# Kernel optimization log

Hardware: AMD Instinct MI355X
Metric: run time of the kernel (lower is better)

Reference implementation:

```python
import jax, jax.numpy as jnp
import numpy as np

EPS = 1e-5

def sage_conv(x, edge_index, w_l, b_l, w_r):
    # PyG SAGEConv with mean aggregation: lin_l(mean of source-neighbor feats per dst) + lin_r(x)
    n = x.shape[0]
    src, dst = edge_index[0], edge_index[1]
    agg = jax.ops.segment_sum(x[src], dst, num_segments=n)  # [N, d]
    deg = jax.ops.segment_sum(jnp.ones((edge_index.shape[1],), x.dtype), dst, num_segments=n)
    agg = agg / jnp.maximum(deg, 1.0)[:, None]
    return agg @ w_l + b_l + x @ w_r

def batchnorm_eval(x, gamma, beta, mean, var):
    return (x - mean) * (gamma * jax.lax.rsqrt(var + EPS)) + beta

def setup_inputs() -> dict:
    key = jax.random.key(0)
    ks = jax.random.split(key, 12)
    N, E, D, H, O = 10000, 160000, 512, 512, 256
    inp = {
        'x': jax.random.normal(ks[0], (N, D), jnp.float32),
        'edge_index': jax.random.randint(ks[1], (2, E), 0, N, jnp.int32),
        'w_l1': jax.random.normal(ks[2], (D, H), jnp.float32) * (1.0 / np.sqrt(D)),
        'b1': jnp.zeros((H,), jnp.float32),
        'w_r1': jax.random.normal(ks[3], (D, H), jnp.float32) * (1.0 / np.sqrt(D)),
        'bn1_gamma': jnp.ones((H,), jnp.float32),
        'bn1_beta': jnp.zeros((H,), jnp.float32),
        'bn1_mean': jax.random.normal(ks[4], (H,), jnp.float32) * 0.1,
        'bn1_var': jax.random.uniform(ks[5], (H,), jnp.float32, 0.5, 1.5),
        'w_l2': jax.random.normal(ks[6], (H, H), jnp.float32) * (1.0 / np.sqrt(H)),
        'b2': jnp.zeros((H,), jnp.float32),
        'w_r2': jax.random.normal(ks[7], (H, H), jnp.float32) * (1.0 / np.sqrt(H)),
        'bn2_gamma': jnp.ones((H,), jnp.float32),
        'bn2_beta': jnp.zeros((H,), jnp.float32),
        'bn2_mean': jax.random.normal(ks[8], (H,), jnp.float32) * 0.1,
        'bn2_var': jax.random.uniform(ks[9], (H,), jnp.float32, 0.5, 1.5),
        'w_l3': jax.random.normal(ks[10], (H, O), jnp.float32) * (1.0 / np.sqrt(H)),
        'b3': jnp.zeros((O,), jnp.float32),
        'w_r3': jax.random.normal(ks[11], (H, O), jnp.float32) * (1.0 / np.sqrt(H)),
    }
    return inp

def reference(x, edge_index, w_l1, b1, w_r1, bn1_gamma, bn1_beta, bn1_mean, bn1_var,
              w_l2, b2, w_r2, bn2_gamma, bn2_beta, bn2_mean, bn2_var,
              w_l3, b3, w_r3):
    # Layer 1: SAGEConv -> BN (eval) -> ReLU (dropout is identity in eval)
    h = sage_conv(x, edge_index, w_l1, b1, w_r1)
    h = jax.nn.relu(batchnorm_eval(h, bn1_gamma, bn1_beta, bn1_mean, bn1_var))
    # Layer 2
    h = sage_conv(h, edge_index, w_l2, b2, w_r2)
    h = jax.nn.relu(batchnorm_eval(h, bn2_gamma, bn2_beta, bn2_mean, bn2_var))
    # Layer 3 (no BN/ReLU)
    return sage_conv(h, edge_index, w_l3, b3, w_r3)
```

## Files before the change

### kernel.cpp

```cpp
#include <hip/hip_runtime.h>

#define NNODE 10000
#define NEDGE 160000

using frag8 = __attribute__((ext_vector_type(8))) short;
using f32x4 = __attribute__((ext_vector_type(4))) float;

__device__ __forceinline__ unsigned short f2bf(float f) {
    union { float f; unsigned u; } v; v.f = f;
    unsigned r = (v.u + 0x7fffu + ((v.u >> 16) & 1u)) >> 16;
    return (unsigned short)r;
}
__device__ __forceinline__ float bf2f(unsigned short s) {
    union { unsigned u; float f; } v; v.u = ((unsigned)s) << 16; return v.f;
}

__global__ __launch_bounds__(1024) void k_scan(const int* __restrict__ deg,
                                               int* __restrict__ rs,
                                               int* __restrict__ cur, int n, int total) {
    const int tid = threadIdx.x;
    const int CH = 10;
    const int base = tid * CH;
    int vals[CH];
    int tsum = 0;
#pragma unroll
    for (int j = 0; j < CH; j++) {
        int v = (base + j < n) ? deg[base + j] : 0;
        vals[j] = v; tsum += v;
    }
    const int lane = tid & 63, wid = tid >> 6;
    int x = tsum;
#pragma unroll
    for (int d = 1; d < 64; d <<= 1) {
        int y = __shfl_up(x, d, 64);
        if (lane >= d) x += y;
    }
    __shared__ int wt[16];
    if (lane == 63) wt[wid] = x;
    __syncthreads();
    if (tid == 0) {
        int c = 0;
#pragma unroll
        for (int k = 0; k < 16; k++) { int t = wt[k]; wt[k] = c; c += t; }
    }
    __syncthreads();
    int run = wt[wid] + x - tsum;
#pragma unroll
    for (int j = 0; j < CH; j++) {
        if (base + j < n) { rs[base + j] = run; cur[base + j] = run; }
        run += vals[j];
    }
    if (tid == 0) rs[n] = total;
}

__global__ void k_fill(const int* __restrict__ src, const int* __restrict__ dst,
                       int E, int* __restrict__ cur, int* __restrict__ csr) {
    int e = blockIdx.x * 256 + threadIdx.x;
    if (e < E) {
        int p = atomicAdd(&cur[dst[e]], 1);
        csr[p] = src[e];
    }
}

__global__ __launch_bounds__(256) void k_prep(
    const float* __restrict__ x, unsigned short* __restrict__ xb,
    const float* __restrict__ wl1, const float* __restrict__ wr1,
    const float* __restrict__ wl2, const float* __restrict__ wr2,
    const float* __restrict__ wl3, const float* __restrict__ wr3,
    unsigned short* __restrict__ bt1, unsigned short* __restrict__ bt2,
    unsigned short* __restrict__ bt3,
    const float* __restrict__ b1, const float* __restrict__ g1, const float* __restrict__ be1,
    const float* __restrict__ m1, const float* __restrict__ v1,
    const float* __restrict__ b2, const float* __restrict__ g2, const float* __restrict__ be2,
    const float* __restrict__ m2, const float* __restrict__ v2,
    const float* __restrict__ b3,
    float* __restrict__ sc1, float* __restrict__ sh1,
    float* __restrict__ sc2, float* __restrict__ sh2,
    float* __restrict__ sc3, float* __restrict__ sh3,
    const int* __restrict__ dstI, int* __restrict__ deg) {
    const int b = blockIdx.x, tid = threadIdx.x;
    if (b < 5000) {
        int i = b * 256 + tid;
        float4 f = ((const float4*)x)[i];
        ushort4 o;
        o.x = f2bf(f.x); o.y = f2bf(f.y); o.z = f2bf(f.z); o.w = f2bf(f.w);
        ((ushort4*)xb)[i] = o;
        return;
    }
    if (b >= 6281) {
        int e = (b - 6281) * 256 + tid;
        if (e < NEDGE) atomicAdd(&deg[dstI[e]], 1);
        return;
    }
    if (b == 6280) {
        for (int t = tid; t < 512; t += 256) {
            float s1 = g1[t] * rsqrtf(v1[t] + 1e-5f);
            sc1[t] = s1; sh1[t] = (b1[t] - m1[t]) * s1 + be1[t];
            float s2 = g2[t] * rsqrtf(v2[t] + 1e-5f);
            sc2[t] = s2; sh2[t] = (b2[t] - m2[t]) * s2 + be2[t];
        }
        if (tid < 256) { sc3[tid] = 1.0f; sh3[tid] = b3[tid]; }
        return;
    }
    __shared__ float t[32][33];
    int tj = b - 5000;
    const float* srcp; unsigned short* dstp; int C, koff, ntilesN;
    if (tj < 1024) {
        int job = tj >> 8; int tile = tj & 255; C = 512; ntilesN = 16;
        srcp = (job == 0) ? wl1 : (job == 1) ? wr1 : (job == 2) ? wl2 : wr2;
        dstp = (job < 2) ? bt1 : bt2; koff = (job & 1) * 512;
        tj = tile;
    } else {
        int jj = tj - 1024; int job = jj >> 7; int tile = jj & 127; C = 256; ntilesN = 8;
        srcp = (job == 0) ? wl3 : wr3; dstp = bt3; koff = job * 512;
        tj = tile;
    }
    int k0 = (tj / ntilesN) * 32, c0 = (tj % ntilesN) * 32;
    int tx = tid & 31, ty = tid >> 5;
#pragma unroll
    for (int q = 0; q < 4; q++)
        t[ty + 8 * q][tx] = srcp[(long)(k0 + ty + 8 * q) * C + c0 + tx];
    __syncthreads();
#pragma unroll
    for (int q = 0; q < 4; q++)
        dstp[(long)(c0 + ty + 8 * q) * 1024 + koff + k0 + tx] = f2bf(t[tx][ty + 8 * q]);
}

__global__ __launch_bounds__(64) void k_agg(const unsigned short* __restrict__ S,
                                            const int* __restrict__ rs, const int* __restrict__ csr,
                                            unsigned short* __restrict__ outb) {
    const int n = blockIdx.x;
    const int c = blockIdx.y * 256 + threadIdx.x * 4;
    const int s = rs[n], e = rs[n + 1];
    float a0 = 0.f, a1 = 0.f, a2 = 0.f, a3 = 0.f;
    int i = s;
    for (; i + 4 <= e; i += 4) {
        int r0 = csr[i], r1 = csr[i + 1], r2 = csr[i + 2], r3 = csr[i + 3];
        uint2 u0 = *(const uint2*)(S + (long)r0 * 512 + c);
        uint2 u1 = *(const uint2*)(S + (long)r1 * 512 + c);
        uint2 u2 = *(const uint2*)(S + (long)r2 * 512 + c);
        uint2 u3 = *(const uint2*)(S + (long)r3 * 512 + c);
        a0 += bf2f((unsigned short)(u0.x & 0xffffu)); a1 += bf2f((unsigned short)(u0.x >> 16));
        a2 += bf2f((unsigned short)(u0.y & 0xffffu)); a3 += bf2f((unsigned short)(u0.y >> 16));
        a0 += bf2f((unsigned short)(u1.x & 0xffffu)); a1 += bf2f((unsigned short)(u1.x >> 16));
        a2 += bf2f((unsigned short)(u1.y & 0xffffu)); a3 += bf2f((unsigned short)(u1.y >> 16));
        a0 += bf2f((unsigned short)(u2.x & 0xffffu)); a1 += bf2f((unsigned short)(u2.x >> 16));
        a2 += bf2f((unsigned short)(u2.y & 0xffffu)); a3 += bf2f((unsigned short)(u2.y >> 16));
        a0 += bf2f((unsigned short)(u3.x & 0xffffu)); a1 += bf2f((unsigned short)(u3.x >> 16));
        a2 += bf2f((unsigned short)(u3.y & 0xffffu)); a3 += bf2f((unsigned short)(u3.y >> 16));
    }
    for (; i < e; i++) {
        uint2 u = *(const uint2*)(S + (long)csr[i] * 512 + c);
        a0 += bf2f((unsigned short)(u.x & 0xffffu)); a1 += bf2f((unsigned short)(u.x >> 16));
        a2 += bf2f((unsigned short)(u.y & 0xffffu)); a3 += bf2f((unsigned short)(u.y >> 16));
    }
    const int cnt = e - s;
    const float inv = 1.f / (float)(cnt > 1 ? cnt : 1);
    uint2 o;
    o.x = (unsigned)f2bf(a0 * inv) | ((unsigned)f2bf(a1 * inv) << 16);
    o.y = (unsigned)f2bf(a2 * inv) | ((unsigned)f2bf(a3 * inv) << 16);
    *(uint2*)(outb + (long)n * 512 + c) = o;
}

template <int MODE, int NOUT>
__global__ __launch_bounds__(256, 2) void k_gemm(const unsigned short* __restrict__ Agg,
                                                 const unsigned short* __restrict__ Self,
                                                 const unsigned short* __restrict__ Bt,
                                                 const float* __restrict__ sc, const float* __restrict__ sh,
                                                 unsigned short* __restrict__ hout, float* __restrict__ fout,
                                                 int M) {
    constexpr int NT = NOUT / 128;
    constexpr int QSH = (NT == 4) ? 5 : 4;
    const int b = blockIdx.x;
    const int X = b & 7;
    const int q = (b >> 3) & (NT - 1);
    const int g = b >> QSH;
    const int m0 = (g * 8 + X) * 128;
    if (m0 >= M) return;
    const int n0 = q * 128;

    __shared__ __align__(16) short As[2][128 * 64];
    __shared__ __align__(16) short Bs[2][128 * 64];
    const int tid = threadIdx.x;
    const int w = tid >> 6, lane = tid & 63;
    const int wm = (w >> 1) * 64, wn = (w & 1) * 64;
    const int fr = lane & 15, fq = lane >> 4, sw = fr & 7;
    const int srow = w * 8 + (lane >> 3);
    const int scol = (((lane & 7) ^ (lane >> 3)) * 8);
    const int ldsOff = w * 8 * 64;

    f32x4 acc[4][4];
#pragma unroll
    for (int i = 0; i < 4; i++)
#pragma unroll
        for (int j = 0; j < 4; j++)
#pragma unroll
            for (int r = 0; r < 4; r++) acc[i][j][r] = 0.f;

    auto issue = [&](int t, int buf) {
        const short* abase = (const short*)((t < 8) ? Agg : Self);
        const int kk = (t & 7) * 64;
        const int k0 = t * 64;
#pragma unroll
        for (int cch = 0; cch < 4; cch++) {
            __builtin_amdgcn_global_load_lds(
                (const __attribute__((address_space(1))) void*)(abase + (long)(m0 + cch * 32 + srow) * 512 + kk + scol),
                (__attribute__((address_space(3))) void*)(&As[buf][ldsOff + cch * 32 * 64]), 16, 0, 0);
            __builtin_amdgcn_global_load_lds(
                (const __attribute__((address_space(1))) void*)((const short*)Bt + (long)(n0 + cch * 32 + srow) * 1024 + k0 + scol),
                (__attribute__((address_space(3))) void*)(&Bs[buf][ldsOff + cch * 32 * 64]), 16, 0, 0);
        }
    };

    issue(0, 0);
#pragma unroll
    for (int t = 0; t < 16; t++) {
        const int cur = t & 1;
        __syncthreads();
        if (t < 15) issue(t + 1, cur ^ 1);
#pragma unroll
        for (int ks = 0; ks < 2; ks++) {
            frag8 af[4], bf[4];
#pragma unroll
            for (int i = 0; i < 4; i++)
                af[i] = *(const frag8*)(&As[cur][(wm + i * 16 + fr) * 64 + (((ks * 4 + fq) ^ sw) * 8)]);
#pragma unroll
            for (int j = 0; j < 4; j++)
                bf[j] = *(const frag8*)(&Bs[cur][(wn + j * 16 + fr) * 64 + (((ks * 4 + fq) ^ sw) * 8)]);
#pragma unroll
            for (int i = 0; i < 4; i++)
#pragma unroll
                for (int j = 0; j < 4; j++)
                    acc[i][j] = __builtin_amdgcn_mfma_f32_16x16x32_bf16(af[i], bf[j], acc[i][j], 0, 0, 0);
        }
    }

    float scj[4], shj[4];
#pragma unroll
    for (int j = 0; j < 4; j++) {
        int col = n0 + wn + j * 16 + fr;
        scj[j] = sc[col]; shj[j] = sh[col];
    }
#pragma unroll
    for (int i = 0; i < 4; i++) {
        int rowb = m0 + wm + i * 16 + fq * 4;
#pragma unroll
        for (int j = 0; j < 4; j++) {
            int col = n0 + wn + j * 16 + fr;
#pragma unroll
            for (int r = 0; r < 4; r++) {
                int row = rowb + r;
                if (row < M) {
                    float y = acc[i][j][r] * scj[j] + shj[j];
                    if constexpr (MODE == 0) {
                        y = fmaxf(y, 0.f);
                        hout[(long)row * 512 + col] = f2bf(y);
                    } else {
                        fout[(long)row * NOUT + col] = y;
                    }
                }
            }
        }
    }
}

extern "C" void kernel_launch(void* const* d_in, const int* in_sizes, int n_in,
                              void* d_out, int out_size, void* d_ws, size_t ws_size,
                              hipStream_t stream) {
    const float* x    = (const float*)d_in[0];
    const int*   ei   = (const int*)d_in[1];
    const float* w_l1 = (const float*)d_in[2];
    const float* b1   = (const float*)d_in[3];
    const float* w_r1 = (const float*)d_in[4];
    const float* g1   = (const float*)d_in[5];
    const float* be1  = (const float*)d_in[6];
    const float* m1   = (const float*)d_in[7];
    const float* v1   = (const float*)d_in[8];
    const float* w_l2 = (const float*)d_in[9];
    const float* b2   = (const float*)d_in[10];
    const float* w_r2 = (const float*)d_in[11];
    const float* g2   = (const float*)d_in[12];
    const float* be2  = (const float*)d_in[13];
    const float* m2   = (const float*)d_in[14];
    const float* v2   = (const float*)d_in[15];
    const float* w_l3 = (const float*)d_in[16];
    const float* b3   = (const float*)d_in[17];
    const float* w_r3 = (const float*)d_in[18];
    float* out = (float*)d_out;

    const int N = NNODE, E = NEDGE;
    const int* srcI = ei;
    const int* dstI = ei + E;

    char* w = (char*)d_ws;
    auto alloc = [&](size_t bytes) { void* p = (void*)w; w += (bytes + 255) & ~(size_t)255; return p; };
    int* deg = (int*)alloc((size_t)N * 4);
    int* rs  = (int*)alloc((size_t)(N + 1) * 4);
    int* cur = (int*)alloc((size_t)N * 4);
    int* csr = (int*)alloc((size_t)E * 4);
    unsigned short* xb   = (unsigned short*)alloc((size_t)N * 512 * 2);
    unsigned short* bt1  = (unsigned short*)alloc((size_t)512 * 1024 * 2);
    unsigned short* bt2  = (unsigned short*)alloc((size_t)512 * 1024 * 2);
    unsigned short* bt3  = (unsigned short*)alloc((size_t)256 * 1024 * 2);
    float* sc1 = (float*)alloc(512 * 4); float* sh1 = (float*)alloc(512 * 4);
    float* sc2 = (float*)alloc(512 * 4); float* sh2 = (float*)alloc(512 * 4);
    float* sc3 = (float*)alloc(256 * 4); float* sh3 = (float*)alloc(256 * 4);
    unsigned short* agg_a = (unsigned short*)alloc((size_t)N * 512 * 2);
    unsigned short* h1    = (unsigned short*)alloc((size_t)N * 512 * 2);
    unsigned short* h2    = (unsigned short*)alloc((size_t)N * 512 * 2);
    (void)alloc(256 * 1024);

    hipMemsetAsync(deg, 0, (size_t)N * 4, stream);
    k_prep<<<6906, 256, 0, stream>>>(x, xb, w_l1, w_r1, w_l2, w_r2, w_l3, w_r3,
                                     bt1, bt2, bt3,
                                     b1, g1, be1, m1, v1, b2, g2, be2, m2, v2, b3,
                                     sc1, sh1, sc2, sh2, sc3, sh3, dstI, deg);
    k_scan<<<1, 1024, 0, stream>>>(deg, rs, cur, N, E);
    k_fill<<<(E + 255) / 256, 256, 0, stream>>>(srcI, dstI, E, cur, csr);

    dim3 ga(N, 2);

    k_agg<<<ga, 64, 0, stream>>>(xb, rs, csr, agg_a);
    k_gemm<0, 512><<<320, 256, 0, stream>>>(agg_a, xb, bt1, sc1, sh1, h1, nullptr, N);
    k_agg<<<ga, 64, 0, stream>>>(h1, rs, csr, agg_a);
    k_gemm<0, 512><<<320, 256, 0, stream>>>(agg_a, h1, bt2, sc2, sh2, h2, nullptr, N);
    k_agg<<<ga, 64, 0, stream>>>(h2, rs, csr, agg_a);
    k_gemm<1, 256><<<160, 256, 0, stream>>>(agg_a, h2, bt3, sc3, sh3, nullptr, out, N);
}
```

Measured before the change: 249.6 us.

## Restructure neighbor aggregation into column-sliced persistent blocks with split-edge waves

Replaces the one-block-per-node, 64-thread aggregation kernel with a grid-strided kernel of 2048 blocks of 256 threads. Each block owns a 64-column slice (X = blockIdx & 7) and processes 4 nodes at a time, one per wave. Within a wave, the two 32-lane halves read alternate neighbours as 4-byte loads and combine their sums with a cross-lane shuffle. Launch overhead and per-block scheduling cost drop, and the column slicing may improve L2 locality for feature rows, but each load is narrower and more edge-index loads are issued per byte.

```diff
diff --git a/kernel.cpp b/kernel.cpp
--- a/kernel.cpp
+++ b/kernel.cpp
@@ -126,40 +126,44 @@
         dstp[(long)(c0 + ty + 8 * q) * 1024 + koff + k0 + tx] = f2bf(t[tx][ty + 8 * q]);
 }
 
-__global__ __launch_bounds__(64) void k_agg(const unsigned short* __restrict__ S,
-                                            const int* __restrict__ rs, const int* __restrict__ csr,
-                                            unsigned short* __restrict__ outb) {
-    const int n = blockIdx.x;
-    const int c = blockIdx.y * 256 + threadIdx.x * 4;
-    const int s = rs[n], e = rs[n + 1];
-    float a0 = 0.f, a1 = 0.f, a2 = 0.f, a3 = 0.f;
-    int i = s;
-    for (; i + 4 <= e; i += 4) {
-        int r0 = csr[i], r1 = csr[i + 1], r2 = csr[i + 2], r3 = csr[i + 3];
-        uint2 u0 = *(const uint2*)(S + (long)r0 * 512 + c);
-        uint2 u1 = *(const uint2*)(S + (long)r1 * 512 + c);
-        uint2 u2 = *(const uint2*)(S + (long)r2 * 512 + c);
-        uint2 u3 = *(const uint2*)(S + (long)r3 * 512 + c);
-        a0 += bf2f((unsigned short)(u0.x & 0xffffu)); a1 += bf2f((unsigned short)(u0.x >> 16));
-        a2 += bf2f((unsigned short)(u0.y & 0xffffu)); a3 += bf2f((unsigned short)(u0.y >> 16));
-        a0 += bf2f((unsigned short)(u1.x & 0xffffu)); a1 += bf2f((unsigned short)(u1.x >> 16));
-        a2 += bf2f((unsigned short)(u1.y & 0xffffu)); a3 += bf2f((unsigned short)(u1.y >> 16));
-        a0 += bf2f((unsigned short)(u2.x & 0xffffu)); a1 += bf2f((unsigned short)(u2.x >> 16));
-        a2 += bf2f((unsigned short)(u2.y & 0xffffu)); a3 += bf2f((unsigned short)(u2.y >> 16));
-        a0 += bf2f((unsigned short)(u3.x & 0xffffu)); a1 += bf2f((unsigned short)(u3.x >> 16));
-        a2 += bf2f((unsigned short)(u3.y & 0xffffu)); a3 += bf2f((unsigned short)(u3.y >> 16));
-    }
-    for (; i < e; i++) {
-        uint2 u = *(const uint2*)(S + (long)csr[i] * 512 + c);
-        a0 += bf2f((unsigned short)(u.x & 0xffffu)); a1 += bf2f((unsigned short)(u.x >> 16));
-        a2 += bf2f((unsigned short)(u.y & 0xffffu)); a3 += bf2f((unsigned short)(u.y >> 16));
-    }
-    const int cnt = e - s;
-    const float inv = 1.f / (float)(cnt > 1 ? cnt : 1);
-    uint2 o;
-    o.x = (unsigned)f2bf(a0 * inv) | ((unsigned)f2bf(a1 * inv) << 16);
-    o.y = (unsigned)f2bf(a2 * inv) | ((unsigned)f2bf(a3 * inv) << 16);
-    *(uint2*)(outb + (long)n * 512 + c) = o;
+__global__ __launch_bounds__(256) void k_agg(const unsigned short* __restrict__ S,
+                                             const int* __restrict__ rs, const int* __restrict__ csr,
+                                             unsigned short* __restrict__ outb) {
+    const int X = blockIdx.x & 7;
+    const int grp = blockIdx.x >> 3;
+    const int wave = threadIdx.x >> 6;
+    const int lane = threadIdx.x & 63;
+    const int half = lane >> 5;
+    const int c = X * 64 + (lane & 31) * 2;
+    for (int n = grp * 4 + wave; n < NNODE; n += 1024) {
+        const int s = rs[n], e = rs[n + 1];
+        float a0 = 0.f, a1 = 0.f;
+        int i = s;
+        for (; i + 4 <= e; i += 4) {
+            int s0 = csr[i + half], s1 = csr[i + 2 + half];
+            unsigned u0 = *(const unsigned*)(S + (long)s0 * 512 + c);
+            unsigned u1 = *(const unsigned*)(S + (long)s1 * 512 + c);
+            a0 += bf2f((unsigned short)(u0 & 0xffffu)) + bf2f((unsigned short)(u1 & 0xffffu));
+            a1 += bf2f((unsigned short)(u0 >> 16)) + bf2f((unsigned short)(u1 >> 16));
+        }
+        for (; i < e; i += 2) {
+            int j = i + half;
+            if (j < e) {
+                int sj = csr[j];
+                unsigned u = *(const unsigned*)(S + (long)sj * 512 + c);
+                a0 += bf2f((unsigned short)(u & 0xffffu));
+                a1 += bf2f((unsigned short)(u >> 16));
+            }
+        }
+        a0 += __shfl_xor(a0, 32, 64);
+        a1 += __shfl_xor(a1, 32, 64);
+        const int cnt = e - s;
+        const float inv = 1.f / (float)(cnt > 1 ? cnt : 1);
+        if (half == 0) {
+            unsigned o = (unsigned)f2bf(a0 * inv) | ((unsigned)f2bf(a1 * inv) << 16);
+            *(unsigned*)(outb + (long)n * 512 + c) = o;
+        }
+    }
 }
 
 template <int MODE, int NOUT>
@@ -318,12 +322,10 @@
     k_scan<<<1, 1024, 0, stream>>>(deg, rs, cur, N, E);
     k_fill<<<(E + 255) / 256, 256, 0, stream>>>(srcI, dstI, E, cur, csr);
 
-    dim3 ga(N, 2);
-
-    k_agg<<<ga, 64, 0, stream>>>(xb, rs, csr, agg_a);
+    k_agg<<<2048, 256, 0, stream>>>(xb, rs, csr, agg_a);
     k_gemm<0, 512><<<320, 256, 0, stream>>>(agg_a, xb, bt1, sc1, sh1, h1, nullptr, N);
-    k_agg<<<ga, 64, 0, stream>>>(h1, rs, csr, agg_a);
+    k_agg<<<2048, 256, 0, stream>>>(h1, rs, csr, agg_a);
     k_gemm<0, 512><<<320, 256, 0, stream>>>(agg_a, h1, bt2, sc2, sh2, h2, nullptr, N);
-    k_agg<<<ga, 64, 0, stream>>>(h2, rs, csr, agg_a);
+    k_agg<<<2048, 256, 0, stream>>>(h2, rs, csr, agg_a);
     k_gemm<1, 256><<<160, 256, 0, stream>>>(agg_a, h2, bt3, sc3, sh3, nullptr, out, N);
 }
```

Measured after the change: 291.4 us. 16.8% more time.
